# Performance work log

Hardware: AMD Instinct MI355X
Metric: run time of the kernel (lower is better)

The kernel has to match this reference:

```python
import jax, jax.numpy as jnp
import numpy as np


def _sdpa(q, k, v):
    # scaled dot-product attention, no dropout (eval mode)
    d = q.shape[-1]
    s = jnp.einsum('bhqd,bhkd->bhqk', q, k) / jnp.sqrt(jnp.asarray(d, q.dtype))
    a = jax.nn.softmax(s, axis=-1)
    return jnp.einsum('bhqk,bhkd->bhqd', a, v)


def setup_inputs() -> dict:
    key = jax.random.key(0)
    ks = jax.random.split(key, 9)
    BC, H, N, d = 128, 4, 1024, 64
    B, C = 4, 32
    C_ch, l, r, TC = 32, 16, 8, 144
    half_dim = H * d  # 256
    q_t = jax.random.normal(ks[0], (BC, H, N, d), jnp.float32)
    k_t = jax.random.normal(ks[1], (BC, H, N, d), jnp.float32)
    v_t = jax.random.normal(ks[2], (BC, H, N, d), jnp.float32)
    L_n = jax.random.normal(ks[3], (B * N, C_ch, C_ch), jnp.float32)
    slots = jax.random.normal(ks[4], (1, l, half_dim), jnp.float32) * 0.02
    pack_q_w = jax.random.normal(ks[5], (half_dim, half_dim), jnp.float32) * 0.02
    mu_proto_factors = jax.random.normal(ks[6], (l, TC, r), jnp.float32) * 0.02
    spd_beta = jnp.array([0.5], jnp.float32)
    channel_idx = jax.random.randint(ks[7], (C_ch,), 0, TC)
    return dict(q_t=q_t, k_t=k_t, v_t=v_t, L_n=L_n, slots=slots,
                pack_q_w=pack_q_w, mu_proto_factors=mu_proto_factors,
                spd_beta=spd_beta, channel_idx=channel_idx, C=C)


def _spd_distances(L_per_sample, mu_proto_factors, channel_idx):
    # L_per_sample: (B, N, C_ch, C_ch) -> distances (B, l, N)
    B, N, C_ch, _ = L_per_sample.shape
    l = mu_proto_factors.shape[0]
    U_sub = mu_proto_factors[:, channel_idx]            # (l, C_ch, r)
    L_flat = L_per_sample.reshape(B, N, C_ch * C_ch)    # (B, N, C_ch^2)
    L_sqnorm = jnp.sum(L_flat * L_flat, axis=-1)        # (B, N)
    UtU = jnp.einsum('lcr,lcs->lrs', U_sub, U_sub)      # (l, r, r)
    mu_sqnorm = jnp.sum(UtU * UtU, axis=(-2, -1))       # (l,)
    mu_sub = jnp.einsum('lcr,ldr->lcd', U_sub, U_sub)   # (l, C_ch, C_ch)
    mu_flat = mu_sub.reshape(l, C_ch * C_ch)
    cross = jnp.einsum('bni,li->bnl', L_flat, mu_flat)  # (B, N, l)
    dist_sq = L_sqnorm[..., None] + mu_sqnorm[None, None, :] - 2.0 * cross
    dist_sq = jnp.clip(dist_sq, 0.0, None)
    return jnp.sqrt(dist_sq).transpose(0, 2, 1)         # (B, l, N)


def reference(q_t, k_t, v_t, L_n, slots, pack_q_w, mu_proto_factors,
              spd_beta, channel_idx, C):
    BC, H, N, d = q_t.shape
    l = slots.shape[1]
    scale = d ** (-0.5)
    # pack queries: Linear(bias=False) then split heads; slots are shared across batch
    pq = slots[0] @ pack_q_w.T                          # (l, H*d)
    pq = pq.reshape(l, H, d).transpose(1, 0, 2)         # (H, l, d)
    pack_score = jnp.einsum('hld,bhnd->bhln', pq, k_t) * scale  # (BC, H, l, N)
    # SPD geometric bias (L_n is detached in the original)
    B = BC // C
    C_ch = L_n.shape[1]
    L_per_sample = jax.lax.stop_gradient(L_n).reshape(B, N, C_ch, C_ch)
    spd_dist_b = _spd_distances(L_per_sample, mu_proto_factors, channel_idx)  # (B, l, N)
    spd_dist = jnp.repeat(spd_dist_b, C, axis=0)        # (BC, l, N)
    pack_score = pack_score - spd_beta[0] * spd_dist[:, None, :, :]
    pack_attn = jax.nn.softmax(pack_score, axis=-1)
    packed = jnp.einsum('bhln,bhnd->bhld', pack_attn, v_t)  # (BC, H, l, d)
    processed = _sdpa(packed, packed, packed)               # (BC, H, l, d)
    out = _sdpa(q_t, processed, processed)                  # (BC, H, N, d)
    return out
```

## Files before the change

### kernel.cpp

```cpp
#include <hip/hip_runtime.h>
#include <hip/hip_bf16.h>

typedef unsigned short ushort_t;

__global__ __launch_bounds__(256) void k_pq(const float* __restrict__ slots,
                                            const float* __restrict__ W,
                                            float* __restrict__ pq) {
    int l = blockIdx.x, j = threadIdx.x;
    __shared__ float SL[256];
    SL[j] = slots[l * 256 + j];
    __syncthreads();
    const float4* wr = (const float4*)(W + j * 256);
    float acc = 0.f;
#pragma unroll 8
    for (int g = 0; g < 64; ++g) {
        float4 wv = wr[g];
        const float* sl = &SL[g * 4];
        acc += wv.x * sl[0] + wv.y * sl[1] + wv.z * sl[2] + wv.w * sl[3];
    }
    int h = j >> 6, d = j & 63;
    pq[(h * 16 + l) * 64 + d] = acc;
}

__global__ void k_mu(const float* __restrict__ mu,
                     const int* __restrict__ cidx,
                     float* __restrict__ mu_flat,
                     float* __restrict__ mu_sq) {
    int l = blockIdx.x;
    __shared__ float U[256];
    __shared__ float utu[64];
    int t = threadIdx.x;
    {
        int c = t >> 3, r = t & 7;
        U[t] = mu[(l * 144 + cidx[c]) * 8 + r];
    }
    __syncthreads();
#pragma unroll
    for (int i = 0; i < 4; ++i) {
        int e = t + i * 256;
        int c = e >> 5, dd = e & 31;
        float acc = 0.f;
#pragma unroll
        for (int r = 0; r < 8; ++r) acc += U[c * 8 + r] * U[dd * 8 + r];
        mu_flat[l * 1024 + e] = acc;
    }
    if (t < 64) {
        int r = t >> 3, s = t & 7;
        float acc = 0.f;
        for (int c = 0; c < 32; ++c) acc += U[c * 8 + r] * U[c * 8 + s];
        utu[t] = acc;
    }
    __syncthreads();
    if (t == 0) {
        float acc = 0.f;
        for (int i = 0; i < 64; ++i) acc += utu[i] * utu[i];
        mu_sq[l] = acc;
    }
}

__global__ __launch_bounds__(256) void k_dist(const float* __restrict__ Ln,
                                              const float* __restrict__ mu_flat,
                                              const float* __restrict__ mu_sq,
                                              float* __restrict__ dist) {
    int blk = blockIdx.x;
    int chunk = blk & 255, bs = blk >> 8;
    int t = threadIdx.x;
    int rid = t >> 6, lane = t & 63;
    int l = lane >> 2, cs = lane & 3;
    int n = chunk * 4 + rid;
    const float4* L4 = (const float4*)(Ln + ((size_t)(bs * 1024 + n)) * 1024) + cs * 64;
    const float4* M4 = (const float4*)mu_flat + l * 256 + cs * 64;
    float cr = 0.f, lsq = 0.f;
#pragma unroll 8
    for (int i = 0; i < 64; ++i) {
        float4 lv = L4[i];
        float4 mv = M4[i];
        cr  += lv.x * mv.x + lv.y * mv.y + lv.z * mv.z + lv.w * mv.w;
        lsq += lv.x * lv.x + lv.y * lv.y + lv.z * lv.z + lv.w * lv.w;
    }
    cr  += __shfl_xor(cr, 1);  cr  += __shfl_xor(cr, 2);
    lsq += __shfl_xor(lsq, 1); lsq += __shfl_xor(lsq, 2);
    if (cs == 0) {
        float d2 = lsq + mu_sq[l] - 2.f * cr;
        dist[((size_t)(bs * 16 + l)) * 1024 + n] = sqrtf(fmaxf(d2, 0.f));
    }
}

__global__ __launch_bounds__(256) void k_score(const float* __restrict__ kt,
                                               const float* __restrict__ pq,
                                               const float* __restrict__ dist,
                                               const float* __restrict__ beta_p,
                                               float* __restrict__ pbuf,
                                               float* __restrict__ psum) {
    int bx = blockIdx.x;
    int nq = bx & 3, bh = bx >> 2;
    int h = bh & 3;
    int bs = bh >> 7;
    __shared__ __align__(16) float PQ[1024];
    __shared__ float wsum[64];
    int t = threadIdx.x;
    int lane = t & 63, w = t >> 6;
    ((float4*)PQ)[t] = ((const float4*)(pq + h * 1024))[t & 255];
    float beta = beta_p[0];
    __syncthreads();

    int n = nq * 256 + t;
    const float4* kr = (const float4*)(kt + ((size_t)bh) * 65536 + (size_t)n * 64);
    float sc[16];
#pragma unroll
    for (int l = 0; l < 16; ++l) sc[l] = 0.f;
#pragma unroll
    for (int gb = 0; gb < 4; ++gb) {
        float4 kv0 = kr[gb * 4 + 0];
        float4 kv1 = kr[gb * 4 + 1];
        float4 kv2 = kr[gb * 4 + 2];
        float4 kv3 = kr[gb * 4 + 3];
#pragma unroll
        for (int l = 0; l < 16; ++l) {
            const float* p = &PQ[l * 64 + gb * 16];
            sc[l] += kv0.x * p[0]  + kv0.y * p[1]  + kv0.z * p[2]  + kv0.w * p[3]
                   + kv1.x * p[4]  + kv1.y * p[5]  + kv1.z * p[6]  + kv1.w * p[7]
                   + kv2.x * p[8]  + kv2.y * p[9]  + kv2.z * p[10] + kv2.w * p[11]
                   + kv3.x * p[12] + kv3.y * p[13] + kv3.z * p[14] + kv3.w * p[15];
        }
    }
#pragma unroll
    for (int l = 0; l < 16; ++l) {
        float e = __expf(0.125f * sc[l] - beta * dist[((size_t)(bs * 16 + l)) * 1024 + n]);
        sc[l] = e;
        pbuf[((size_t)(bh * 16 + l)) * 1024 + n] = e;
    }
#pragma unroll
    for (int l = 0; l < 16; ++l) {
        float s = sc[l];
#pragma unroll
        for (int off = 32; off >= 1; off >>= 1) s += __shfl_xor(s, off);
        if (lane == 0) wsum[l * 4 + w] = s;
    }
    __syncthreads();
    if (t < 16)
        psum[((size_t)(bh * 16 + t)) * 4 + nq] =
            wsum[t * 4 + 0] + wsum[t * 4 + 1] + wsum[t * 4 + 2] + wsum[t * 4 + 3];
}

__global__ __launch_bounds__(1024) void k_pv(const float* __restrict__ vt,
                                             const float* __restrict__ pbuf,
                                             const float* __restrict__ psum,
                                             float* __restrict__ packed) {
    int bh = blockIdx.x;
    __shared__ __align__(16) float RED[4096];
    int t = threadIdx.x;
    int lane = t & 63, w = t >> 6;
    int jg = w >> 2;
    int sl = (w & 3) * 4 + (lane >> 4);
    int dg = lane & 15;
    const float4* pb4 = (const float4*)(pbuf + ((size_t)(bh * 16 + sl)) * 1024 + jg * 256);
    const float4* v4  = (const float4*)(vt + ((size_t)bh) * 65536) + (size_t)(jg * 256) * 16 + dg;
    float4 acc; acc.x = acc.y = acc.z = acc.w = 0.f;
    for (int rb = 0; rb < 32; ++rb) {
        float4 pA = pb4[rb * 2 + 0];
        float4 pB = pb4[rb * 2 + 1];
        float4 v0 = v4[(rb * 8 + 0) * 16];
        float4 v1 = v4[(rb * 8 + 1) * 16];
        float4 v2 = v4[(rb * 8 + 2) * 16];
        float4 v3 = v4[(rb * 8 + 3) * 16];
        float4 v5 = v4[(rb * 8 + 4) * 16];
        float4 v6 = v4[(rb * 8 + 5) * 16];
        float4 v7 = v4[(rb * 8 + 6) * 16];
        float4 v8 = v4[(rb * 8 + 7) * 16];
        acc.x += pA.x * v0.x + pA.y * v1.x + pA.z * v2.x + pA.w * v3.x
               + pB.x * v5.x + pB.y * v6.x + pB.z * v7.x + pB.w * v8.x;
        acc.y += pA.x * v0.y + pA.y * v1.y + pA.z * v2.y + pA.w * v3.y
               + pB.x * v5.y + pB.y * v6.y + pB.z * v7.y + pB.w * v8.y;
        acc.z += pA.x * v0.z + pA.y * v1.z + pA.z * v2.z + pA.w * v3.z
               + pB.x * v5.z + pB.y * v6.z + pB.z * v7.z + pB.w * v8.z;
        acc.w += pA.x * v0.w + pA.y * v1.w + pA.z * v2.w + pA.w * v3.w
               + pB.x * v5.w + pB.y * v6.w + pB.z * v7.w + pB.w * v8.w;
    }
    ((float4*)RED)[jg * 256 + sl * 16 + dg] = acc;
    __syncthreads();
    int l = t >> 6, d = t & 63;
    float S = psum[((size_t)(bh * 16 + l)) * 4 + 0] + psum[((size_t)(bh * 16 + l)) * 4 + 1]
            + psum[((size_t)(bh * 16 + l)) * 4 + 2] + psum[((size_t)(bh * 16 + l)) * 4 + 3];
    float sum = RED[l * 64 + d] + RED[1024 + l * 64 + d]
              + RED[2048 + l * 64 + d] + RED[3072 + l * 64 + d];
    packed[((size_t)bh) * 1024 + t] = sum / S;
}

__global__ void k_proc(const float* __restrict__ packed, float* __restrict__ proc) {
    int bh = blockIdx.x;
    __shared__ float P[1024];
    __shared__ float A[256];
    int t = threadIdx.x;
#pragma unroll
    for (int i = 0; i < 4; ++i) P[t + i * 256] = packed[(size_t)bh * 1024 + t + i * 256];
    __syncthreads();
    {
        int i = t >> 4, j = t & 15;
        float acc = 0.f;
#pragma unroll
        for (int dd = 0; dd < 64; ++dd) acc += P[i * 64 + dd] * P[j * 64 + dd];
        A[t] = acc * 0.125f;
    }
    __syncthreads();
    if (t < 16) {
        float m = -1e30f;
#pragma unroll
        for (int j = 0; j < 16; ++j) m = fmaxf(m, A[t * 16 + j]);
        float s = 0.f;
#pragma unroll
        for (int j = 0; j < 16; ++j) { float e = __expf(A[t * 16 + j] - m); A[t * 16 + j] = e; s += e; }
        float inv = 1.f / s;
#pragma unroll
        for (int j = 0; j < 16; ++j) A[t * 16 + j] *= inv;
    }
    __syncthreads();
#pragma unroll
    for (int i = 0; i < 4; ++i) {
        int e = t + i * 256;
        int r = e >> 6, d = e & 63;
        float acc = 0.f;
#pragma unroll
        for (int j = 0; j < 16; ++j) acc += A[r * 16 + j] * P[j * 64 + d];
        proc[(size_t)bh * 1024 + e] = acc;
    }
}

__global__ __launch_bounds__(256) void k_final(const float* __restrict__ qt,
                                               const float* __restrict__ proc,
                                               float* __restrict__ out) {
    int bh = blockIdx.x >> 3, chunk = blockIdx.x & 7;
    __shared__ __align__(16) float P[1024];
    int t = threadIdx.x;
    ((float4*)P)[t] = ((const float4*)(proc + (size_t)bh * 1024))[t];
    __syncthreads();
    int q = t & 3, rid = t >> 2;
    int n0 = chunk * 128 + rid, n1 = n0 + 64;
    const float4* q0 = (const float4*)(qt + ((size_t)bh * 1024 + n0) * 64) + q * 4;
    const float4* q1 = (const float4*)(qt + ((size_t)bh * 1024 + n1) * 64) + q * 4;
    float4 qa0 = q0[0], qa1 = q0[1], qa2 = q0[2], qa3 = q0[3];
    float4 qb0 = q1[0], qb1 = q1[1], qb2 = q1[2], qb3 = q1[3];
    const float4* P4 = (const float4*)P + q * 4;

    float s0[16], s1[16];
#pragma unroll
    for (int j = 0; j < 16; ++j) {
        float4 p0 = P4[j * 16 + 0], p1 = P4[j * 16 + 1];
        float4 p2 = P4[j * 16 + 2], p3 = P4[j * 16 + 3];
        float a = qa0.x * p0.x + qa0.y * p0.y + qa0.z * p0.z + qa0.w * p0.w
                + qa1.x * p1.x + qa1.y * p1.y + qa1.z * p1.z + qa1.w * p1.w
                + qa2.x * p2.x + qa2.y * p2.y + qa2.z * p2.z + qa2.w * p2.w
                + qa3.x * p3.x + qa3.y * p3.y + qa3.z * p3.z + qa3.w * p3.w;
        float b = qb0.x * p0.x + qb0.y * p0.y + qb0.z * p0.z + qb0.w * p0.w
                + qb1.x * p1.x + qb1.y * p1.y + qb1.z * p1.z + qb1.w * p1.w
                + qb2.x * p2.x + qb2.y * p2.y + qb2.z * p2.z + qb2.w * p2.w
                + qb3.x * p3.x + qb3.y * p3.y + qb3.z * p3.z + qb3.w * p3.w;
        a += __shfl_xor(a, 1); a += __shfl_xor(a, 2);
        b += __shfl_xor(b, 1); b += __shfl_xor(b, 2);
        s0[j] = a * 0.125f; s1[j] = b * 0.125f;
    }
    float m0 = s0[0], m1 = s1[0];
#pragma unroll
    for (int j = 1; j < 16; ++j) { m0 = fmaxf(m0, s0[j]); m1 = fmaxf(m1, s1[j]); }
    float t0 = 0.f, t1 = 0.f;
#pragma unroll
    for (int j = 0; j < 16; ++j) {
        s0[j] = __expf(s0[j] - m0); t0 += s0[j];
        s1[j] = __expf(s1[j] - m1); t1 += s1[j];
    }
    float i0 = 1.f / t0, i1 = 1.f / t1;
#pragma unroll
    for (int j = 0; j < 16; ++j) { s0[j] *= i0; s1[j] *= i1; }

    float4 o00, o01, o02, o03, o10, o11, o12, o13;
    o00.x=o00.y=o00.z=o00.w=0.f; o01=o00; o02=o00; o03=o00;
    o10=o00; o11=o00; o12=o00; o13=o00;
#pragma unroll
    for (int j = 0; j < 16; ++j) {
        float4 p0 = P4[j * 16 + 0], p1 = P4[j * 16 + 1];
        float4 p2 = P4[j * 16 + 2], p3 = P4[j * 16 + 3];
        float a = s0[j], b = s1[j];
        o00.x += a * p0.x; o00.y += a * p0.y; o00.z += a * p0.z; o00.w += a * p0.w;
        o01.x += a * p1.x; o01.y += a * p1.y; o01.z += a * p1.z; o01.w += a * p1.w;
        o02.x += a * p2.x; o02.y += a * p2.y; o02.z += a * p2.z; o02.w += a * p2.w;
        o03.x += a * p3.x; o03.y += a * p3.y; o03.z += a * p3.z; o03.w += a * p3.w;
        o10.x += b * p0.x; o10.y += b * p0.y; o10.z += b * p0.z; o10.w += b * p0.w;
        o11.x += b * p1.x; o11.y += b * p1.y; o11.z += b * p1.z; o11.w += b * p1.w;
        o12.x += b * p2.x; o12.y += b * p2.y; o12.z += b * p2.z; o12.w += b * p2.w;
        o13.x += b * p3.x; o13.y += b * p3.y; o13.z += b * p3.z; o13.w += b * p3.w;
    }
    float4* w0 = (float4*)(out + ((size_t)bh * 1024 + n0) * 64) + q * 4;
    float4* w1 = (float4*)(out + ((size_t)bh * 1024 + n1) * 64) + q * 4;
    w0[0] = o00; w0[1] = o01; w0[2] = o02; w0[3] = o03;
    w1[0] = o10; w1[1] = o11; w1[2] = o12; w1[3] = o13;
}

extern "C" void kernel_launch(void* const* d_in, const int* in_sizes, int n_in,
                              void* d_out, int out_size, void* d_ws, size_t ws_size,
                              hipStream_t stream) {
    const float* q     = (const float*)d_in[0];
    const float* k     = (const float*)d_in[1];
    const float* v     = (const float*)d_in[2];
    const float* Ln    = (const float*)d_in[3];
    const float* slots = (const float*)d_in[4];
    const float* W     = (const float*)d_in[5];
    const float* mu    = (const float*)d_in[6];
    const float* beta  = (const float*)d_in[7];
    const int* cidx    = (const int*)d_in[8];

    float* ws     = (float*)d_ws;
    float* pq     = ws;
    float* muf    = ws + 4096;
    float* musq   = ws + 20480;
    float* dist   = ws + 20496;
    float* packed = ws + 86032;
    float* proc   = ws + 610320;
    float* psum   = ws + 1134608;
    const size_t WS_NEEDED = (size_t)(1167376 + 8388608) * sizeof(float);
    float* pbuf   = (ws_size >= WS_NEEDED) ? (ws + 1167376) : (float*)d_out;

    k_pq   <<<16,   256, 0, stream>>>(slots, W, pq);
    k_mu   <<<16,   256, 0, stream>>>(mu, cidx, muf, musq);
    k_dist <<<1024, 256, 0, stream>>>(Ln, muf, musq, dist);
    k_score<<<2048, 256, 0, stream>>>(k, pq, dist, beta, pbuf, psum);
    k_pv   <<<512, 1024, 0, stream>>>(v, pbuf, psum, packed);
    k_proc <<<512,  256, 0, stream>>>(packed, proc);
    k_final<<<4096, 256, 0, stream>>>(q, proc, (float*)d_out);
}
```

Before: 640.0 us.

## Split PV reduction across four blocks per head and restructure score loads

```diff
diff --git a/kernel.cpp b/kernel.cpp
--- a/kernel.cpp
+++ b/kernel.cpp
@@ -86,12 +86,12 @@
     }
 }
 
-__global__ __launch_bounds__(256) void k_score(const float* __restrict__ kt,
-                                               const float* __restrict__ pq,
-                                               const float* __restrict__ dist,
-                                               const float* __restrict__ beta_p,
-                                               float* __restrict__ pbuf,
-                                               float* __restrict__ psum) {
+__global__ __launch_bounds__(256, 4) void k_score(const float* __restrict__ kt,
+                                                  const float* __restrict__ pq,
+                                                  const float* __restrict__ dist,
+                                                  const float* __restrict__ beta_p,
+                                                  float* __restrict__ pbuf,
+                                                  float* __restrict__ psum) {
     int bx = blockIdx.x;
     int nq = bx & 3, bh = bx >> 2;
     int h = bh & 3;
@@ -102,31 +102,43 @@
     int lane = t & 63, w = t >> 6;
     ((float4*)PQ)[t] = ((const float4*)(pq + h * 1024))[t & 255];
     float beta = beta_p[0];
-    __syncthreads();
-
     int n = nq * 256 + t;
+
+    float dd[16];
+#pragma unroll
+    for (int l = 0; l < 16; ++l) dd[l] = dist[((size_t)(bs * 16 + l)) * 1024 + n];
+    __syncthreads();
+
     const float4* kr = (const float4*)(kt + ((size_t)bh) * 65536 + (size_t)n * 64);
     float sc[16];
 #pragma unroll
     for (int l = 0; l < 16; ++l) sc[l] = 0.f;
-#pragma unroll
-    for (int gb = 0; gb < 4; ++gb) {
-        float4 kv0 = kr[gb * 4 + 0];
-        float4 kv1 = kr[gb * 4 + 1];
-        float4 kv2 = kr[gb * 4 + 2];
-        float4 kv3 = kr[gb * 4 + 3];
-#pragma unroll
-        for (int l = 0; l < 16; ++l) {
-            const float* p = &PQ[l * 64 + gb * 16];
-            sc[l] += kv0.x * p[0]  + kv0.y * p[1]  + kv0.z * p[2]  + kv0.w * p[3]
-                   + kv1.x * p[4]  + kv1.y * p[5]  + kv1.z * p[6]  + kv1.w * p[7]
-                   + kv2.x * p[8]  + kv2.y * p[9]  + kv2.z * p[10] + kv2.w * p[11]
-                   + kv3.x * p[12] + kv3.y * p[13] + kv3.z * p[14] + kv3.w * p[15];
-        }
-    }
+    float4 kv[8];
+#pragma unroll
+    for (int j = 0; j < 8; ++j) kv[j] = kr[j];
 #pragma unroll
     for (int l = 0; l < 16; ++l) {
-        float e = __expf(0.125f * sc[l] - beta * dist[((size_t)(bs * 16 + l)) * 1024 + n]);
+        const float* p = &PQ[l * 64];
+        float s = 0.f;
+#pragma unroll
+        for (int j = 0; j < 8; ++j)
+            s += kv[j].x * p[j*4] + kv[j].y * p[j*4+1] + kv[j].z * p[j*4+2] + kv[j].w * p[j*4+3];
+        sc[l] = s;
+    }
+#pragma unroll
+    for (int j = 0; j < 8; ++j) kv[j] = kr[8 + j];
+#pragma unroll
+    for (int l = 0; l < 16; ++l) {
+        const float* p = &PQ[l * 64 + 32];
+        float s = sc[l];
+#pragma unroll
+        for (int j = 0; j < 8; ++j)
+            s += kv[j].x * p[j*4] + kv[j].y * p[j*4+1] + kv[j].z * p[j*4+2] + kv[j].w * p[j*4+3];
+        sc[l] = s;
+    }
+#pragma unroll
+    for (int l = 0; l < 16; ++l) {
+        float e = __expf(0.125f * sc[l] - beta * dd[l]);
         sc[l] = e;
         pbuf[((size_t)(bh * 16 + l)) * 1024 + n] = e;
     }
@@ -143,57 +155,90 @@
             wsum[t * 4 + 0] + wsum[t * 4 + 1] + wsum[t * 4 + 2] + wsum[t * 4 + 3];
 }
 
-__global__ __launch_bounds__(1024) void k_pv(const float* __restrict__ vt,
-                                             const float* __restrict__ pbuf,
-                                             const float* __restrict__ psum,
-                                             float* __restrict__ packed) {
+__global__ __launch_bounds__(256, 4) void k_pv(const float* __restrict__ vt,
+                                               const float* __restrict__ pbuf,
+                                               float* __restrict__ pp) {
+    int bx = blockIdx.x;
+    int ng = bx & 3, bh = bx >> 2;
+    __shared__ __align__(16) float PT[16 * 256];
+    __shared__ __align__(16) float RED[4 * 1024];
+    int t = threadIdx.x;
+    int lane = t & 63, w = t >> 6;
+#pragma unroll
+    for (int i = 0; i < 4; ++i) {
+        int e4 = t + i * 256;
+        ((float4*)PT)[e4] =
+            ((const float4*)pbuf)[((size_t)(bh * 16 + (e4 >> 6))) * 256 + ng * 64 + (e4 & 63)];
+    }
+    __syncthreads();
+
+    int sg = lane >> 4, dg = lane & 15;
+    int R0 = ng * 256 + w * 64;
+    const float4* vb = (const float4*)vt + (size_t)bh * 16384;
+    float4 acc[16];
+#pragma unroll
+    for (int sl = 0; sl < 16; ++sl) { acc[sl].x = acc[sl].y = acc[sl].z = acc[sl].w = 0.f; }
+
+    float4 v0 = vb[(R0 + 0 * 4 + sg) * 16 + dg];
+    float4 v1 = vb[(R0 + 1 * 4 + sg) * 16 + dg];
+    for (int rg = 0; rg < 16; ++rg) {
+        float4 v2;
+        if (rg < 14) v2 = vb[(R0 + (rg + 2) * 4 + sg) * 16 + dg];
+        const float* pr = &PT[w * 64 + rg * 4 + sg];
+#pragma unroll
+        for (int sl = 0; sl < 16; ++sl) {
+            float p = pr[sl * 256];
+            acc[sl].x += p * v0.x; acc[sl].y += p * v0.y;
+            acc[sl].z += p * v0.z; acc[sl].w += p * v0.w;
+        }
+        v0 = v1; v1 = v2;
+    }
+#pragma unroll
+    for (int sl = 0; sl < 16; ++sl) {
+        acc[sl].x += __shfl_xor(acc[sl].x, 16); acc[sl].x += __shfl_xor(acc[sl].x, 32);
+        acc[sl].y += __shfl_xor(acc[sl].y, 16); acc[sl].y += __shfl_xor(acc[sl].y, 32);
+        acc[sl].z += __shfl_xor(acc[sl].z, 16); acc[sl].z += __shfl_xor(acc[sl].z, 32);
+        acc[sl].w += __shfl_xor(acc[sl].w, 16); acc[sl].w += __shfl_xor(acc[sl].w, 32);
+    }
+    if (lane < 16) {
+#pragma unroll
+        for (int sl = 0; sl < 16; ++sl)
+            ((float4*)RED)[w * 256 + sl * 16 + lane] = acc[sl];
+    }
+    __syncthreads();
+    float4 s0 = ((float4*)RED)[t];
+    float4 s1 = ((float4*)RED)[256 + t];
+    float4 s2 = ((float4*)RED)[512 + t];
+    float4 s3 = ((float4*)RED)[768 + t];
+    float4 sum;
+    sum.x = s0.x + s1.x + s2.x + s3.x;
+    sum.y = s0.y + s1.y + s2.y + s3.y;
+    sum.z = s0.z + s1.z + s2.z + s3.z;
+    sum.w = s0.w + s1.w + s2.w + s3.w;
+    ((float4*)pp)[(size_t)bx * 256 + t] = sum;
+}
+
+__global__ void k_proc(const float* __restrict__ pp,
+                       const float* __restrict__ psum,
+                       float* __restrict__ proc) {
     int bh = blockIdx.x;
-    __shared__ __align__(16) float RED[4096];
-    int t = threadIdx.x;
-    int lane = t & 63, w = t >> 6;
-    int jg = w >> 2;
-    int sl = (w & 3) * 4 + (lane >> 4);
-    int dg = lane & 15;
-    const float4* pb4 = (const float4*)(pbuf + ((size_t)(bh * 16 + sl)) * 1024 + jg * 256);
-    const float4* v4  = (const float4*)(vt + ((size_t)bh) * 65536) + (size_t)(jg * 256) * 16 + dg;
-    float4 acc; acc.x = acc.y = acc.z = acc.w = 0.f;
-    for (int rb = 0; rb < 32; ++rb) {
-        float4 pA = pb4[rb * 2 + 0];
-        float4 pB = pb4[rb * 2 + 1];
-        float4 v0 = v4[(rb * 8 + 0) * 16];
-        float4 v1 = v4[(rb * 8 + 1) * 16];
-        float4 v2 = v4[(rb * 8 + 2) * 16];
-        float4 v3 = v4[(rb * 8 + 3) * 16];
-        float4 v5 = v4[(rb * 8 + 4) * 16];
-        float4 v6 = v4[(rb * 8 + 5) * 16];
-        float4 v7 = v4[(rb * 8 + 6) * 16];
-        float4 v8 = v4[(rb * 8 + 7) * 16];
-        acc.x += pA.x * v0.x + pA.y * v1.x + pA.z * v2.x + pA.w * v3.x
-               + pB.x * v5.x + pB.y * v6.x + pB.z * v7.x + pB.w * v8.x;
-        acc.y += pA.x * v0.y + pA.y * v1.y + pA.z * v2.y + pA.w * v3.y
-               + pB.x * v5.y + pB.y * v6.y + pB.z * v7.y + pB.w * v8.y;
-        acc.z += pA.x * v0.z + pA.y * v1.z + pA.z * v2.z + pA.w * v3.z
-               + pB.x * v5.z + pB.y * v6.z + pB.z * v7.z + pB.w * v8.z;
-        acc.w += pA.x * v0.w + pA.y * v1.w + pA.z * v2.w + pA.w * v3.w
-               + pB.x * v5.w + pB.y * v6.w + pB.z * v7.w + pB.w * v8.w;
-    }
-    ((float4*)RED)[jg * 256 + sl * 16 + dg] = acc;
-    __syncthreads();
-    int l = t >> 6, d = t & 63;
-    float S = psum[((size_t)(bh * 16 + l)) * 4 + 0] + psum[((size_t)(bh * 16 + l)) * 4 + 1]
-            + psum[((size_t)(bh * 16 + l)) * 4 + 2] + psum[((size_t)(bh * 16 + l)) * 4 + 3];
-    float sum = RED[l * 64 + d] + RED[1024 + l * 64 + d]
-              + RED[2048 + l * 64 + d] + RED[3072 + l * 64 + d];
-    packed[((size_t)bh) * 1024 + t] = sum / S;
-}
-
-__global__ void k_proc(const float* __restrict__ packed, float* __restrict__ proc) {
-    int bh = blockIdx.x;
-    __shared__ float P[1024];
+    __shared__ __align__(16) float P[1024];
     __shared__ float A[256];
     int t = threadIdx.x;
-#pragma unroll
-    for (int i = 0; i < 4; ++i) P[t + i * 256] = packed[(size_t)bh * 1024 + t + i * 256];
+    {
+        int sl = t >> 4;
+        const float* ps = &psum[((size_t)(bh * 16 + sl)) * 4];
+        float S = ps[0] + ps[1] + ps[2] + ps[3];
+        float inv = 1.f / S;
+        const float4* p4 = (const float4*)pp + (size_t)(bh * 4) * 256 + t;
+        float4 a = p4[0], b = p4[256], c = p4[512], d = p4[768];
+        float4 r;
+        r.x = (a.x + b.x + c.x + d.x) * inv;
+        r.y = (a.y + b.y + c.y + d.y) * inv;
+        r.z = (a.z + b.z + c.z + d.z) * inv;
+        r.w = (a.w + b.w + c.w + d.w) * inv;
+        ((float4*)P)[t] = r;
+    }
     __syncthreads();
     {
         int i = t >> 4, j = t & 15;
@@ -313,17 +358,23 @@
     float* muf    = ws + 4096;
     float* musq   = ws + 20480;
     float* dist   = ws + 20496;
-    float* packed = ws + 86032;
-    float* proc   = ws + 610320;
-    float* psum   = ws + 1134608;
-    const size_t WS_NEEDED = (size_t)(1167376 + 8388608) * sizeof(float);
-    float* pbuf   = (ws_size >= WS_NEEDED) ? (ws + 1167376) : (float*)d_out;
+    float* proc   = ws + 86032;
+    float* psum   = ws + 610320;
+    const size_t WS_NEEDED = (size_t)(643088 + 8388608 + 2097152) * sizeof(float);
+    float* pbuf, * pp;
+    if (ws_size >= WS_NEEDED) {
+        pbuf = ws + 643088;
+        pp   = ws + 643088 + 8388608;
+    } else {
+        pbuf = (float*)d_out;
+        pp   = (float*)d_out + 8388608;
+    }
 
     k_pq   <<<16,   256, 0, stream>>>(slots, W, pq);
     k_mu   <<<16,   256, 0, stream>>>(mu, cidx, muf, musq);
     k_dist <<<1024, 256, 0, stream>>>(Ln, muf, musq, dist);
     k_score<<<2048, 256, 0, stream>>>(k, pq, dist, beta, pbuf, psum);
-    k_pv   <<<512, 1024, 0, stream>>>(v, pbuf, psum, packed);
-    k_proc <<<512,  256, 0, stream>>>(packed, proc);
+    k_pv   <<<2048, 256, 0, stream>>>(v, pbuf, pp);
+    k_proc <<<512,  256, 0, stream>>>(pp, psum, proc);
     k_final<<<4096, 256, 0, stream>>>(q, proc, (float*)d_out);
 }
```

Result: faster. 584.0 us (-8.7%).
